# Kernel tuning notes

Measured on AMD Instinct MI355X. Metric: run time of the kernel, lower is better.

## Reference

```python
import jax, jax.numpy as jnp
import numpy as np

B, S, D = 4, 2048, 1024

def setup_inputs() -> dict:
    key = jax.random.key(0)
    ks = jax.random.split(key, 7)
    sc = 1.0 / np.sqrt(D)
    return {
        "x": jax.random.normal(ks[0], (B, S, D), dtype=jnp.float32),
        "Wq": jax.random.normal(ks[1], (D, D), dtype=jnp.float32) * sc,
        "bq": jax.random.normal(ks[2], (D,), dtype=jnp.float32) * 0.01,
        "Wk": jax.random.normal(ks[3], (D, D), dtype=jnp.float32) * sc,
        "bk": jax.random.normal(ks[4], (D,), dtype=jnp.float32) * 0.01,
        "Wv": jax.random.normal(ks[5], (D, D), dtype=jnp.float32) * sc,
        "bv": jax.random.normal(ks[6], (D,), dtype=jnp.float32) * 0.01,
    }

def reference(x, Wq, bq, Wk, bk, Wv, bv):
    # q, k, v: [B, S, D] projections (torch Linear: x @ W^T + b; here W stored as [in, out])
    q = jnp.einsum("bsd,df->bsf", x, Wq) + bq
    k = jnp.einsum("bsd,df->bsf", x, Wk) + bk
    v = jnp.einsum("bsd,df->bsf", x, Wv) + bv
    dim = x.shape[-1]
    # scores: [B, S, S], scaled by sqrt(full d_model) as in the source
    scores = jnp.einsum("bqd,bkd->bqk", q, k) / jnp.sqrt(jnp.float32(dim)).astype(x.dtype)
    attn = jax.nn.softmax(scores, axis=-1)
    return jnp.einsum("bqk,bkd->bqd", attn, v)
```

## Files before the change

### kernel.cpp

```cpp
#include <hip/hip_runtime.h>
#include <hip/hip_bf16.h>

typedef __attribute__((ext_vector_type(8))) short bf16x8;
typedef __attribute__((ext_vector_type(4))) float f32x4;
typedef unsigned short u16;

__device__ __forceinline__ u16 f2bf(float f) {
  unsigned int u = __builtin_bit_cast(unsigned int, f);
  u += 0x7fffu + ((u >> 16) & 1u);
  return (u16)(u >> 16);
}
__device__ __forceinline__ float bf2f(unsigned int h) {
  unsigned int u = h << 16;
  return __builtin_bit_cast(float, u);
}

__device__ __forceinline__ void gload_lds16(const void* g, void* l) {
  __builtin_amdgcn_global_load_lds(
      (const __attribute__((address_space(1))) void*)g,
      (__attribute__((address_space(3))) void*)l, 16, 0, 0);
}

#define BAR() __builtin_amdgcn_s_barrier()
#define VMC(N) asm volatile("s_waitcnt vmcnt(%0)" ::"n"(N) : "memory")

template <int EPI>
__global__ __launch_bounds__(512, 2) void gemm8x(
    const u16* __restrict__ Abase, const u16* __restrict__ Btbase,
    const float* __restrict__ bq, const float* __restrict__ bk,
    const float* __restrict__ bv, void* __restrict__ out0,
    void* __restrict__ out1, void* __restrict__ out2, int Kd, int ldc,
    long long sAz, long long sBz, long long sCz) {
  constexpr int HSZ = 16384;
  constexpr int BUFSZ = 4 * HSZ;
  __shared__ char lds[2 * BUFSZ];

  const int tid = threadIdx.x;
  const int w = tid >> 6, l = tid & 63;
  const int wr = w >> 2, wc = w & 3;
  const int lq = l >> 4, lr = l & 15;
  const int bm = blockIdx.y * 256, bn = blockIdx.x * 256;
  const int z = blockIdx.z;
  const u16* A = Abase + (size_t)z * sAz;
  const u16* Bt = Btbase + (size_t)z * sBz;
  const int NTk = Kd >> 6;

  const int kbp = ((tid & 7) ^ ((tid >> 3) & 7)) * 8;
  const int drow = tid >> 3;
  const u16* gA[2][2];
  const u16* gB[2][2];
#pragma unroll
  for (int h = 0; h < 2; ++h)
#pragma unroll
    for (int u = 0; u < 2; ++u) {
      gA[h][u] = A + (size_t)(bm + h * 128 + u * 64 + drow) * Kd + kbp;
      gB[h][u] = Bt + (size_t)(bn + h * 128 + u * 64 + drow) * Kd + kbp;
    }

  auto stageA = [&](int buf, int h, int kt) {
    char* d = lds + buf * BUFSZ + h * HSZ + tid * 16;
    gload_lds16(gA[h][0] + kt * 64, d);
    gload_lds16(gA[h][1] + kt * 64, d + 8192);
  };
  auto stageB = [&](int buf, int h, int kt) {
    char* d = lds + buf * BUFSZ + (2 + h) * HSZ + tid * 16;
    gload_lds16(gB[h][0] + kt * 64, d);
    gload_lds16(gB[h][1] + kt * 64, d + 8192);
  };

  const int rA = wr * 64 + lr;
  const int rB = wc * 32 + lr;
  int aoff[2], boff[2];
#pragma unroll
  for (int kh = 0; kh < 2; ++kh) {
    aoff[kh] = rA * 128 + (((kh * 4 + lq) ^ (rA & 7)) << 4);
    boff[kh] = rB * 128 + (((kh * 4 + lq) ^ (rB & 7)) << 4);
  }

  f32x4 acc[2][4][2][2] = {};
  bf16x8 aE[2][4], aO[2][4];
  bf16x8 bb[2][2][2];

#define RD_AE(BUF)                                                        \
  {                                                                       \
    const char* p_ = lds + (BUF)*BUFSZ;                                   \
    _Pragma("unroll") for (int kh = 0; kh < 2; ++kh)                      \
        _Pragma("unroll") for (int mf = 0; mf < 4; ++mf) aE[kh][mf] =     \
            *(const bf16x8*)(p_ + aoff[kh] + mf * 2048);                  \
  }
#define RD_AO(BUF)                                                        \
  {                                                                       \
    const char* p_ = lds + (BUF)*BUFSZ + HSZ;                             \
    _Pragma("unroll") for (int kh = 0; kh < 2; ++kh)                      \
        _Pragma("unroll") for (int mf = 0; mf < 4; ++mf) aO[kh][mf] =     \
            *(const bf16x8*)(p_ + aoff[kh] + mf * 2048);                  \
  }
#define RD_B(BUF, NQ)                                                     \
  {                                                                       \
    const char* p_ = lds + (BUF)*BUFSZ + (2 + (NQ)) * HSZ;                \
    _Pragma("unroll") for (int kh = 0; kh < 2; ++kh)                      \
        _Pragma("unroll") for (int nf = 0; nf < 2; ++nf) bb[NQ][kh][nf] = \
            *(const bf16x8*)(p_ + boff[kh] + nf * 2048);                  \
  }
#define MMAQ(MQ, NQ, ASET)                                                    \
  {                                                                           \
    __builtin_amdgcn_s_setprio(1);                                            \
    _Pragma("unroll") for (int kh = 0; kh < 2; ++kh)                          \
        _Pragma("unroll") for (int mf = 0; mf < 4; ++mf)                      \
            _Pragma("unroll") for (int nf = 0; nf < 2; ++nf) acc[MQ][mf][NQ]  \
                [nf] = __builtin_amdgcn_mfma_f32_16x16x32_bf16(               \
                    ASET[kh][mf], bb[NQ][kh][nf], acc[MQ][mf][NQ][nf], 0, 0,  \
                    0);                                                       \
    __builtin_amdgcn_s_setprio(0);                                            \
  }

  stageA(0, 0, 0);
  stageB(0, 0, 0);
  stageB(0, 1, 0);
  stageA(0, 1, 0);
  stageA(1, 0, 1);
  stageB(1, 0, 1);
  stageB(1, 1, 1);
  VMC(6);
  BAR();

  for (int t = 0; t < NTk; ++t) {
    const int buf = t & 1;
    const bool deep = (t + 2 < NTk);
    if (deep) VMC(6); else VMC(0);
    RD_AE(buf);
    RD_B(buf, 0);
    RD_B(buf, 1);
    if (t + 1 < NTk) stageA(buf ^ 1, 1, t + 1);
    BAR();
    MMAQ(0, 0, aE);
    if (deep) VMC(6); else VMC(0);
    RD_AO(buf);
    if (deep) stageA(buf, 0, t + 2);
    BAR();
    MMAQ(0, 1, aE);
    if (deep) VMC(6); else VMC(0);
    if (deep) stageB(buf, 0, t + 2);
    BAR();
    MMAQ(1, 1, aO);
    if (deep) VMC(6); else VMC(0);
    if (deep) stageB(buf, 1, t + 2);
    BAR();
    MMAQ(1, 0, aO);
  }

  u16* C = (u16*)out0 + (size_t)z * sCz;
#pragma unroll
  for (int nq = 0; nq < 2; ++nq)
#pragma unroll
    for (int nf = 0; nf < 2; ++nf) {
      const int col = bn + wc * 32 + nq * 128 + nf * 16 + lr;
#pragma unroll
      for (int mq = 0; mq < 2; ++mq)
#pragma unroll
        for (int mf = 0; mf < 4; ++mf) {
          const int row = bm + wr * 64 + mq * 128 + mf * 16 + lq * 4;
#pragma unroll
          for (int e = 0; e < 4; ++e)
            C[(size_t)(row + e) * ldc + col] = f2bf(acc[mq][mf][nq][nf][e]);
        }
    }
#undef RD_AE
#undef RD_AO
#undef RD_B
#undef MMAQ
}

template <int EPI>
__global__ __launch_bounds__(512, 2) void gemm2t(
    const u16* __restrict__ Abase, const u16* __restrict__ Btbase,
    const float* __restrict__ bq, const float* __restrict__ bk,
    const float* __restrict__ bv, void* __restrict__ out0,
    void* __restrict__ out1, void* __restrict__ out2, int Kd, int ldc,
    long long sAz, long long sBz, long long sCz) {
  constexpr int ASZ = 16384;
  constexpr int BSZ = 32768;
  constexpr int BBASE = 2 * ASZ;
  __shared__ char lds[2 * ASZ + 3 * BSZ];

  const int tid = threadIdx.x;
  const int w = tid >> 6, l = tid & 63;
  const int wr = w >> 2, wc = w & 3;
  const int lq = l >> 4, lr = l & 15;
  const int bm = blockIdx.y * 128, bn = blockIdx.x * 256;
  const int z = blockIdx.z;
  const u16* A = Abase + (size_t)z * sAz;
  const u16* Bt = Btbase + (size_t)z * sBz;
  const int NT = Kd >> 6;

  const int kbp = ((tid & 7) ^ ((tid >> 3) & 7)) * 8;
  const int drow = tid >> 3;
  const u16* gA[2];
  const u16* gB[4];
#pragma unroll
  for (int u = 0; u < 2; ++u)
    gA[u] = A + (size_t)(bm + u * 64 + drow) * Kd + kbp;
#pragma unroll
  for (int u = 0; u < 4; ++u)
    gB[u] = Bt + (size_t)(bn + u * 64 + drow) * Kd + kbp;

  auto stageA = [&](int kt) {
    char* d = lds + (kt & 1) * ASZ + tid * 16;
#pragma unroll
    for (int u = 0; u < 2; ++u) gload_lds16(gA[u] + kt * 64, d + u * 8192);
  };
  auto stageB = [&](int kt) {
    char* d = lds + BBASE + (kt % 3) * BSZ + tid * 16;
#pragma unroll
    for (int u = 0; u < 4; ++u) gload_lds16(gB[u] + kt * 64, d + u * 8192);
  };

  const int rA = wr * 64 + lr;
  const int rB0 = wc * 64 + lr;
  int aoff[2];
#pragma unroll
  for (int kh = 0; kh < 2; ++kh)
    aoff[kh] = rA * 128 + (((kh * 4 + lq) ^ (rA & 7)) << 4);

  f32x4 acc[4][2][2] = {};
  bf16x8 a[2][4];
  bf16x8 bb[2][2][2];

  auto rdA = [&](int kt) {
    const char* p = lds + (kt & 1) * ASZ;
#pragma unroll
    for (int kh = 0; kh < 2; ++kh)
#pragma unroll
      for (int mf = 0; mf < 4; ++mf)
        a[kh][mf] = *(const bf16x8*)(p + aoff[kh] + mf * 2048);
  };
  auto rdB = [&](int kt) {
    const char* p = lds + BBASE + (kt % 3) * BSZ;
#pragma unroll
    for (int nh = 0; nh < 2; ++nh) {
      const int rB = rB0 + nh * 32;
#pragma unroll
      for (int kh = 0; kh < 2; ++kh) {
        const int o = rB * 128 + (((kh * 4 + lq) ^ (rB & 7)) << 4);
#pragma unroll
        for (int nf = 0; nf < 2; ++nf)
          bb[nh][kh][nf] = *(const bf16x8*)(p + o + nf * 2048);
      }
    }
  };
  auto mma = [&](int kh) {
    __builtin_amdgcn_s_setprio(1);
#pragma unroll
    for (int nh = 0; nh < 2; ++nh)
#pragma unroll
      for (int mf = 0; mf < 4; ++mf)
#pragma unroll
        for (int nf = 0; nf < 2; ++nf)
          acc[mf][nh][nf] = __builtin_amdgcn_mfma_f32_16x16x32_bf16(
              a[kh][mf], bb[nh][kh][nf], acc[mf][nh][nf], 0, 0, 0);
    __builtin_amdgcn_s_setprio(0);
  };

  stageB(0);
  stageA(0);
  stageB(1);
  stageA(1);
  VMC(6);
  BAR();

  for (int t = 0; t < NT; ++t) {
    rdA(t);
    rdB(t);
    if (t + 2 < NT) stageB(t + 2);
    BAR();
    mma(0);
    if (t + 2 < NT) VMC(4); else VMC(0);
    BAR();
    if (t + 2 < NT) stageA(t + 2);
    mma(1);
  }

  if constexpr (EPI == 0) {
    const int mat = bn >> 10;
    const float sc = (mat == 0) ? 0.03125f : 1.0f;
    const float* bias = (mat == 0) ? bq : (mat == 1 ? bk : bv);
    u16* Q = (u16*)out0;
    u16* K = (u16*)out1;
    u16* V = (u16*)out2;
#pragma unroll
    for (int nh = 0; nh < 2; ++nh)
#pragma unroll
      for (int nf = 0; nf < 2; ++nf) {
        const int oc = (bn + wc * 64 + nh * 32 + nf * 16 + lr) & 1023;
        const float bb2 = bias[oc];
#pragma unroll
        for (int mf = 0; mf < 4; ++mf) {
          const int row = bm + wr * 64 + mf * 16 + lq * 4;
          if (mat < 2) {
            u16* dst = (mat == 0) ? Q : K;
#pragma unroll
            for (int e = 0; e < 4; ++e)
              dst[(size_t)(row + e) * 1024 + oc] =
                  f2bf((acc[mf][nh][nf][e] + bb2) * sc);
          } else {
            const int bz = row >> 11, sdx = row & 2047;
            ushort4 pk;
            pk.x = f2bf(acc[mf][nh][nf][0] + bb2);
            pk.y = f2bf(acc[mf][nh][nf][1] + bb2);
            pk.z = f2bf(acc[mf][nh][nf][2] + bb2);
            pk.w = f2bf(acc[mf][nh][nf][3] + bb2);
            *(ushort4*)&V[((size_t)bz * 1024 + oc) * 2048 + sdx] = pk;
          }
        }
      }
  } else {
    float* C = (float*)out0 + (size_t)z * sCz;
#pragma unroll
    for (int nh = 0; nh < 2; ++nh)
#pragma unroll
      for (int nf = 0; nf < 2; ++nf) {
        const int col = bn + wc * 64 + nh * 32 + nf * 16 + lr;
#pragma unroll
        for (int mf = 0; mf < 4; ++mf) {
          const int row = bm + wr * 64 + mf * 16 + lq * 4;
#pragma unroll
          for (int e = 0; e < 4; ++e)
            C[(size_t)(row + e) * ldc + col] = acc[mf][nh][nf][e];
        }
      }
  }
}

__global__ __launch_bounds__(256) void cvt_x(const float* __restrict__ in,
                                             u16* __restrict__ out) {
  const int i = blockIdx.x * 256 + threadIdx.x;
  const float4 v = ((const float4*)in)[i];
  ushort4 o;
  o.x = f2bf(v.x);
  o.y = f2bf(v.y);
  o.z = f2bf(v.z);
  o.w = f2bf(v.w);
  ((ushort4*)out)[i] = o;
}

__global__ void cvt_wt(const float* __restrict__ Wq,
                       const float* __restrict__ Wk,
                       const float* __restrict__ Wv, u16* __restrict__ Wt) {
  __shared__ float s[32][33];
  const float* W = blockIdx.z == 0 ? Wq : (blockIdx.z == 1 ? Wk : Wv);
  u16* O = Wt + (size_t)blockIdx.z * 1048576;
  const int k0 = blockIdx.y * 32, n0 = blockIdx.x * 32;
  s[threadIdx.y][threadIdx.x] =
      W[(size_t)(k0 + threadIdx.y) * 1024 + n0 + threadIdx.x];
  __syncthreads();
  O[(size_t)(n0 + threadIdx.y) * 1024 + k0 + threadIdx.x] =
      f2bf(s[threadIdx.x][threadIdx.y]);
}

__global__ __launch_bounds__(256) void softmax_rows(u16* __restrict__ SP) {
  const size_t base = ((size_t)blockIdx.y * 2048 + blockIdx.x) * 2048;
  u16* p = SP + base;
  const int t = threadIdx.x;
  __shared__ float red[4];

  uint4 u = ((const uint4*)p)[t];
  unsigned int uu[4] = {u.x, u.y, u.z, u.w};
  float f[8];
#pragma unroll
  for (int j = 0; j < 4; ++j) {
    f[2 * j] = bf2f(uu[j] & 0xffffu);
    f[2 * j + 1] = __builtin_bit_cast(float, uu[j] & 0xffff0000u);
  }
  float mx = f[0];
#pragma unroll
  for (int i = 1; i < 8; ++i) mx = fmaxf(mx, f[i]);
#pragma unroll
  for (int o = 32; o; o >>= 1) mx = fmaxf(mx, __shfl_xor(mx, o, 64));
  if ((t & 63) == 0) red[t >> 6] = mx;
  __syncthreads();
  mx = fmaxf(fmaxf(red[0], red[1]), fmaxf(red[2], red[3]));
  __syncthreads();

  float e[8];
  float sum = 0.f;
#pragma unroll
  for (int i = 0; i < 8; ++i) {
    e[i] = __expf(f[i] - mx);
    sum += e[i];
  }
#pragma unroll
  for (int o = 32; o; o >>= 1) sum += __shfl_xor(sum, o, 64);
  if ((t & 63) == 0) red[t >> 6] = sum;
  __syncthreads();
  sum = red[0] + red[1] + red[2] + red[3];
  const float inv = 1.0f / sum;

  uint4 ov;
  unsigned int w0[4];
#pragma unroll
  for (int j = 0; j < 4; ++j) {
    unsigned int lo = f2bf(e[2 * j] * inv);
    unsigned int hi = f2bf(e[2 * j + 1] * inv);
    w0[j] = lo | (hi << 16);
  }
  ov.x = w0[0];
  ov.y = w0[1];
  ov.z = w0[2];
  ov.w = w0[3];
  ((uint4*)p)[t] = ov;
}

extern "C" void kernel_launch(void* const* d_in, const int* in_sizes, int n_in,
                              void* d_out, int out_size, void* d_ws,
                              size_t ws_size, hipStream_t stream) {
  const float* x = (const float*)d_in[0];
  const float* Wq = (const float*)d_in[1];
  const float* bq = (const float*)d_in[2];
  const float* Wk = (const float*)d_in[3];
  const float* bk = (const float*)d_in[4];
  const float* Wv = (const float*)d_in[5];
  const float* bv = (const float*)d_in[6];
  float* out = (float*)d_out;
  char* ws = (char*)d_ws;

  u16* xb = (u16*)ws;
  u16* Wt = (u16*)(ws + 16777216);
  u16* Qb = (u16*)(ws + 23068672);
  u16* Kb = Qb + 8388608;
  u16* Vt = Kb + 8388608;
  u16* SP = Vt + 8388608;

  cvt_x<<<8192, 256, 0, stream>>>(x, xb);
  cvt_wt<<<dim3(32, 32, 3), dim3(32, 32), 0, stream>>>(Wq, Wk, Wv, Wt);

  gemm2t<0><<<dim3(12, 64, 1), 512, 0, stream>>>(
      xb, Wt, bq, bk, bv, Qb, Kb, Vt, 1024, 0, 0, 0, 0);

  gemm8x<2><<<dim3(8, 8, 4), 512, 0, stream>>>(
      Qb, Kb, nullptr, nullptr, nullptr, SP, nullptr, nullptr, 1024, 2048,
      2097152LL, 2097152LL, 4194304LL);

  softmax_rows<<<dim3(2048, 4), 256, 0, stream>>>(SP);

  gemm2t<3><<<dim3(4, 16, 4), 512, 0, stream>>>(
      SP, Vt, nullptr, nullptr, nullptr, out, nullptr, nullptr, 2048, 1024,
      4194304LL, 2097152LL, 2097152LL);
}
```

Measured before the change: 175.8 us.

## Replace large-tile GEMMs with unified 128x128 four-wave kernel for all three GEMMs

```diff
diff --git a/kernel.cpp b/kernel.cpp
--- a/kernel.cpp
+++ b/kernel.cpp
@@ -25,169 +25,22 @@
 #define VMC(N) asm volatile("s_waitcnt vmcnt(%0)" ::"n"(N) : "memory")
 
 template <int EPI>
-__global__ __launch_bounds__(512, 2) void gemm8x(
-    const u16* __restrict__ Abase, const u16* __restrict__ Btbase,
-    const float* __restrict__ bq, const float* __restrict__ bk,
-    const float* __restrict__ bv, void* __restrict__ out0,
-    void* __restrict__ out1, void* __restrict__ out2, int Kd, int ldc,
-    long long sAz, long long sBz, long long sCz) {
-  constexpr int HSZ = 16384;
-  constexpr int BUFSZ = 4 * HSZ;
-  __shared__ char lds[2 * BUFSZ];
-
-  const int tid = threadIdx.x;
-  const int w = tid >> 6, l = tid & 63;
-  const int wr = w >> 2, wc = w & 3;
-  const int lq = l >> 4, lr = l & 15;
-  const int bm = blockIdx.y * 256, bn = blockIdx.x * 256;
-  const int z = blockIdx.z;
-  const u16* A = Abase + (size_t)z * sAz;
-  const u16* Bt = Btbase + (size_t)z * sBz;
-  const int NTk = Kd >> 6;
-
-  const int kbp = ((tid & 7) ^ ((tid >> 3) & 7)) * 8;
-  const int drow = tid >> 3;
-  const u16* gA[2][2];
-  const u16* gB[2][2];
-#pragma unroll
-  for (int h = 0; h < 2; ++h)
-#pragma unroll
-    for (int u = 0; u < 2; ++u) {
-      gA[h][u] = A + (size_t)(bm + h * 128 + u * 64 + drow) * Kd + kbp;
-      gB[h][u] = Bt + (size_t)(bn + h * 128 + u * 64 + drow) * Kd + kbp;
-    }
-
-  auto stageA = [&](int buf, int h, int kt) {
-    char* d = lds + buf * BUFSZ + h * HSZ + tid * 16;
-    gload_lds16(gA[h][0] + kt * 64, d);
-    gload_lds16(gA[h][1] + kt * 64, d + 8192);
-  };
-  auto stageB = [&](int buf, int h, int kt) {
-    char* d = lds + buf * BUFSZ + (2 + h) * HSZ + tid * 16;
-    gload_lds16(gB[h][0] + kt * 64, d);
-    gload_lds16(gB[h][1] + kt * 64, d + 8192);
-  };
-
-  const int rA = wr * 64 + lr;
-  const int rB = wc * 32 + lr;
-  int aoff[2], boff[2];
-#pragma unroll
-  for (int kh = 0; kh < 2; ++kh) {
-    aoff[kh] = rA * 128 + (((kh * 4 + lq) ^ (rA & 7)) << 4);
-    boff[kh] = rB * 128 + (((kh * 4 + lq) ^ (rB & 7)) << 4);
-  }
-
-  f32x4 acc[2][4][2][2] = {};
-  bf16x8 aE[2][4], aO[2][4];
-  bf16x8 bb[2][2][2];
-
-#define RD_AE(BUF)                                                        \
-  {                                                                       \
-    const char* p_ = lds + (BUF)*BUFSZ;                                   \
-    _Pragma("unroll") for (int kh = 0; kh < 2; ++kh)                      \
-        _Pragma("unroll") for (int mf = 0; mf < 4; ++mf) aE[kh][mf] =     \
-            *(const bf16x8*)(p_ + aoff[kh] + mf * 2048);                  \
-  }
-#define RD_AO(BUF)                                                        \
-  {                                                                       \
-    const char* p_ = lds + (BUF)*BUFSZ + HSZ;                             \
-    _Pragma("unroll") for (int kh = 0; kh < 2; ++kh)                      \
-        _Pragma("unroll") for (int mf = 0; mf < 4; ++mf) aO[kh][mf] =     \
-            *(const bf16x8*)(p_ + aoff[kh] + mf * 2048);                  \
-  }
-#define RD_B(BUF, NQ)                                                     \
-  {                                                                       \
-    const char* p_ = lds + (BUF)*BUFSZ + (2 + (NQ)) * HSZ;                \
-    _Pragma("unroll") for (int kh = 0; kh < 2; ++kh)                      \
-        _Pragma("unroll") for (int nf = 0; nf < 2; ++nf) bb[NQ][kh][nf] = \
-            *(const bf16x8*)(p_ + boff[kh] + nf * 2048);                  \
-  }
-#define MMAQ(MQ, NQ, ASET)                                                    \
-  {                                                                           \
-    __builtin_amdgcn_s_setprio(1);                                            \
-    _Pragma("unroll") for (int kh = 0; kh < 2; ++kh)                          \
-        _Pragma("unroll") for (int mf = 0; mf < 4; ++mf)                      \
-            _Pragma("unroll") for (int nf = 0; nf < 2; ++nf) acc[MQ][mf][NQ]  \
-                [nf] = __builtin_amdgcn_mfma_f32_16x16x32_bf16(               \
-                    ASET[kh][mf], bb[NQ][kh][nf], acc[MQ][mf][NQ][nf], 0, 0,  \
-                    0);                                                       \
-    __builtin_amdgcn_s_setprio(0);                                            \
-  }
-
-  stageA(0, 0, 0);
-  stageB(0, 0, 0);
-  stageB(0, 1, 0);
-  stageA(0, 1, 0);
-  stageA(1, 0, 1);
-  stageB(1, 0, 1);
-  stageB(1, 1, 1);
-  VMC(6);
-  BAR();
-
-  for (int t = 0; t < NTk; ++t) {
-    const int buf = t & 1;
-    const bool deep = (t + 2 < NTk);
-    if (deep) VMC(6); else VMC(0);
-    RD_AE(buf);
-    RD_B(buf, 0);
-    RD_B(buf, 1);
-    if (t + 1 < NTk) stageA(buf ^ 1, 1, t + 1);
-    BAR();
-    MMAQ(0, 0, aE);
-    if (deep) VMC(6); else VMC(0);
-    RD_AO(buf);
-    if (deep) stageA(buf, 0, t + 2);
-    BAR();
-    MMAQ(0, 1, aE);
-    if (deep) VMC(6); else VMC(0);
-    if (deep) stageB(buf, 0, t + 2);
-    BAR();
-    MMAQ(1, 1, aO);
-    if (deep) VMC(6); else VMC(0);
-    if (deep) stageB(buf, 1, t + 2);
-    BAR();
-    MMAQ(1, 0, aO);
-  }
-
-  u16* C = (u16*)out0 + (size_t)z * sCz;
-#pragma unroll
-  for (int nq = 0; nq < 2; ++nq)
-#pragma unroll
-    for (int nf = 0; nf < 2; ++nf) {
-      const int col = bn + wc * 32 + nq * 128 + nf * 16 + lr;
-#pragma unroll
-      for (int mq = 0; mq < 2; ++mq)
-#pragma unroll
-        for (int mf = 0; mf < 4; ++mf) {
-          const int row = bm + wr * 64 + mq * 128 + mf * 16 + lq * 4;
-#pragma unroll
-          for (int e = 0; e < 4; ++e)
-            C[(size_t)(row + e) * ldc + col] = f2bf(acc[mq][mf][nq][nf][e]);
-        }
-    }
-#undef RD_AE
-#undef RD_AO
-#undef RD_B
-#undef MMAQ
-}
-
-template <int EPI>
-__global__ __launch_bounds__(512, 2) void gemm2t(
+__global__ __launch_bounds__(256) void gemm2s(
     const u16* __restrict__ Abase, const u16* __restrict__ Btbase,
     const float* __restrict__ bq, const float* __restrict__ bk,
     const float* __restrict__ bv, void* __restrict__ out0,
     void* __restrict__ out1, void* __restrict__ out2, int Kd, int ldc,
     long long sAz, long long sBz, long long sCz) {
   constexpr int ASZ = 16384;
-  constexpr int BSZ = 32768;
+  constexpr int BSZ = 16384;
   constexpr int BBASE = 2 * ASZ;
   __shared__ char lds[2 * ASZ + 3 * BSZ];
 
   const int tid = threadIdx.x;
   const int w = tid >> 6, l = tid & 63;
-  const int wr = w >> 2, wc = w & 3;
+  const int wr = w >> 1, wc = w & 1;
   const int lq = l >> 4, lr = l & 15;
-  const int bm = blockIdx.y * 128, bn = blockIdx.x * 256;
+  const int bm = blockIdx.y * 128, bn = blockIdx.x * 128;
   const int z = blockIdx.z;
   const u16* A = Abase + (size_t)z * sAz;
   const u16* Bt = Btbase + (size_t)z * sBz;
@@ -195,24 +48,23 @@
 
   const int kbp = ((tid & 7) ^ ((tid >> 3) & 7)) * 8;
   const int drow = tid >> 3;
-  const u16* gA[2];
+  const u16* gA[4];
   const u16* gB[4];
 #pragma unroll
-  for (int u = 0; u < 2; ++u)
-    gA[u] = A + (size_t)(bm + u * 64 + drow) * Kd + kbp;
-#pragma unroll
-  for (int u = 0; u < 4; ++u)
-    gB[u] = Bt + (size_t)(bn + u * 64 + drow) * Kd + kbp;
+  for (int u = 0; u < 4; ++u) {
+    gA[u] = A + (size_t)(bm + u * 32 + drow) * Kd + kbp;
+    gB[u] = Bt + (size_t)(bn + u * 32 + drow) * Kd + kbp;
+  }
 
   auto stageA = [&](int kt) {
     char* d = lds + (kt & 1) * ASZ + tid * 16;
 #pragma unroll
-    for (int u = 0; u < 2; ++u) gload_lds16(gA[u] + kt * 64, d + u * 8192);
+    for (int u = 0; u < 4; ++u) gload_lds16(gA[u] + kt * 64, d + u * 4096);
   };
   auto stageB = [&](int kt) {
     char* d = lds + BBASE + (kt % 3) * BSZ + tid * 16;
 #pragma unroll
-    for (int u = 0; u < 4; ++u) gload_lds16(gB[u] + kt * 64, d + u * 8192);
+    for (int u = 0; u < 4; ++u) gload_lds16(gB[u] + kt * 64, d + u * 4096);
   };
 
   const int rA = wr * 64 + lr;
@@ -265,7 +117,7 @@
   stageA(0);
   stageB(1);
   stageA(1);
-  VMC(6);
+  VMC(8);
   BAR();
 
   for (int t = 0; t < NT; ++t) {
@@ -313,6 +165,21 @@
           }
         }
       }
+  } else if constexpr (EPI == 2) {
+    u16* C = (u16*)out0 + (size_t)z * sCz;
+#pragma unroll
+    for (int nh = 0; nh < 2; ++nh)
+#pragma unroll
+      for (int nf = 0; nf < 2; ++nf) {
+        const int col = bn + wc * 64 + nh * 32 + nf * 16 + lr;
+#pragma unroll
+        for (int mf = 0; mf < 4; ++mf) {
+          const int row = bm + wr * 64 + mf * 16 + lq * 4;
+#pragma unroll
+          for (int e = 0; e < 4; ++e)
+            C[(size_t)(row + e) * ldc + col] = f2bf(acc[mf][nh][nf][e]);
+        }
+      }
   } else {
     float* C = (float*)out0 + (size_t)z * sCz;
 #pragma unroll
@@ -433,16 +300,16 @@
   cvt_x<<<8192, 256, 0, stream>>>(x, xb);
   cvt_wt<<<dim3(32, 32, 3), dim3(32, 32), 0, stream>>>(Wq, Wk, Wv, Wt);
 
-  gemm2t<0><<<dim3(12, 64, 1), 512, 0, stream>>>(
+  gemm2s<0><<<dim3(24, 64, 1), 256, 0, stream>>>(
       xb, Wt, bq, bk, bv, Qb, Kb, Vt, 1024, 0, 0, 0, 0);
 
-  gemm8x<2><<<dim3(8, 8, 4), 512, 0, stream>>>(
+  gemm2s<2><<<dim3(16, 16, 4), 256, 0, stream>>>(
       Qb, Kb, nullptr, nullptr, nullptr, SP, nullptr, nullptr, 1024, 2048,
       2097152LL, 2097152LL, 4194304LL);
 
   softmax_rows<<<dim3(2048, 4), 256, 0, stream>>>(SP);
 
-  gemm2t<3><<<dim3(4, 16, 4), 512, 0, stream>>>(
+  gemm2s<3><<<dim3(8, 16, 4), 256, 0, stream>>>(
       SP, Vt, nullptr, nullptr, nullptr, out, nullptr, nullptr, 2048, 1024,
       4194304LL, 2097152LL, 2097152LL);
 }
```

Result: no change. 175.8 us (-0.0%).
